# Kernel optimization log

Measured on AMD Instinct MI355X. Metric: run time of the kernel, lower is better.

Reference implementation:

```python
import jax, jax.numpy as jnp
import numpy as np

B, L, N, F, H, HOR = 32, 12, 1024, 2, 128, 12


def setup_inputs() -> dict:
    key = jax.random.key(0)
    ks = jax.random.split(key, 9)
    x = jax.random.normal(ks[0], (B, L, N, F), dtype=jnp.float32)
    # A_phys: sparse-ish binary physical adjacency, then normalize_adj: add self-loops, row-normalize
    A_phys = (jax.random.uniform(ks[1], (N, N)) < 0.05).astype(jnp.float32)
    A = A_phys + jnp.eye(N, dtype=jnp.float32)
    A = A / (A.sum(axis=1, keepdims=True) + 1e-6)
    # GraphGRUCell params (single layer): lin_x: F -> 3H, lin_h: H -> 3H
    sx = 1.0 / np.sqrt(F)
    sh = 1.0 / np.sqrt(H)
    W_x = jax.random.uniform(ks[2], (F, 3 * H), minval=-sx, maxval=sx)
    b_x = jax.random.uniform(ks[3], (3 * H,), minval=-sx, maxval=sx)
    W_h = jax.random.uniform(ks[4], (H, 3 * H), minval=-sh, maxval=sh)
    b_h = jax.random.uniform(ks[5], (3 * H,), minval=-sh, maxval=sh)
    # head: H -> horizon
    W_head = jax.random.uniform(ks[6], (H, HOR), minval=-sh, maxval=sh)
    b_head = jax.random.uniform(ks[7], (HOR,), minval=-sh, maxval=sh)
    return {"x": x, "A": A, "W_x": W_x, "b_x": b_x, "W_h": W_h, "b_h": b_h,
            "W_head": W_head, "b_head": b_head}


def reference(x, A, W_x, b_x, W_h, b_h, W_head, b_head):
    Bv, Lv, Nv, Fv = x.shape
    Hv = W_h.shape[0]

    def step(h, xt):
        # graph aggregation of hidden state: [N,N] x [B,N,H] -> [B,N,H]
        Ah = jnp.einsum('ij,bjh->bih', A, h)
        x_gates = xt @ W_x + b_x          # [B,N,3H]
        h_gates = Ah @ W_h + b_h          # [B,N,3H]
        z_x, r_x, n_x = jnp.split(x_gates, 3, axis=-1)
        z_h, r_h, n_h = jnp.split(h_gates, 3, axis=-1)
        z = jax.nn.sigmoid(z_x + z_h)
        r = jax.nn.sigmoid(r_x + r_h)
        n = jnp.tanh(n_x + r * n_h)
        h_new = (1.0 - z) * n + z * h
        return h_new, None

    h0 = jnp.zeros((Bv, Nv, Hv), dtype=x.dtype)
    xs = jnp.moveaxis(x, 1, 0)  # [L,B,N,F]
    h, _ = jax.lax.scan(step, h0, xs)
    y = (h @ W_head + b_head).transpose(0, 2, 1)  # [B, horizon, N]
    return y
```

## Files before the change

### kernel.cpp

```cpp
#include <hip/hip_runtime.h>
#include <hip/hip_bf16.h>

#define BB 32
#define LL 12
#define NN 1024
#define HH 128
#define HORN 12
#define G3 384

typedef unsigned short u16;
typedef unsigned int u32;
typedef unsigned long long u64;
typedef __attribute__((ext_vector_type(8))) short short8;
typedef __attribute__((ext_vector_type(4))) float f32x4;

__device__ __forceinline__ u16 to_bf16(float f) {
    return __builtin_bit_cast(u16, __float2bfloat16(f));
}
__device__ __forceinline__ float bf_to_f(u32 bits) {
    return __builtin_bit_cast(float, bits << 16);
}
__device__ __forceinline__ void gl16(const u16* g, char* l) {
    __builtin_amdgcn_global_load_lds((const __attribute__((address_space(1))) u32*)g,
                                     (__attribute__((address_space(3))) u32*)l, 16, 0, 0);
}

__global__ void prep_abf(const float* __restrict__ A, u16* __restrict__ Abf) {
    int t = blockIdx.x * blockDim.x + threadIdx.x;
    float4 v = ((const float4*)A)[t];
    ushort4 o;
    o.x = to_bf16(v.x); o.y = to_bf16(v.y); o.z = to_bf16(v.z); o.w = to_bf16(v.w);
    ((ushort4*)Abf)[t] = o;
}

__global__ void prep_whT(const float* __restrict__ W_h, u16* __restrict__ whT) {
    int t = blockIdx.x * blockDim.x + threadIdx.x;
    if (t >= HH * G3) return;
    int c = t / HH, k = t % HH;
    whT[c * HH + k] = to_bf16(W_h[k * G3 + c]);
}

template <bool FIRST, bool LAST>
__global__ __launch_bounds__(256, 3) void gru_step(
    const u16* __restrict__ Abf, const u16* __restrict__ hT_old,
    u16* __restrict__ hT_new, const u16* __restrict__ whT,
    const float* __restrict__ x, const float* __restrict__ W_x,
    const float* __restrict__ b_x, const float* __restrict__ b_h,
    const float* __restrict__ W_head, const float* __restrict__ b_head,
    float* __restrict__ out, int t) {
    __shared__ __align__(16) char smem[49152];

    int bid = blockIdx.x;
    int swz = (bid & 7) * 64 + (bid >> 3);
    int b = swz >> 4;
    int i0 = (swz & 15) * 64;
    int tid = threadIdx.x;
    int w = tid >> 6, lane = tid & 63;
    int lcol = lane & 15, kgrp = lane >> 4;
    int wm = w >> 1, wn = w & 1;
    u32 swzl = (u32)((lcol & 7) << 4);
    u32 a_b = (u32)((wm * 32 + lcol) * 128);
    u32 b_b = (u32)(8192 + (wn * 64 + lcol) * 128);

    f32x4 acc[2][4];
#pragma unroll
    for (int m = 0; m < 2; ++m)
#pragma unroll
        for (int n = 0; n < 4; ++n) acc[m][n] = (f32x4){0.f, 0.f, 0.f, 0.f};
    u64 hreg[2][4] = {{0, 0, 0, 0}, {0, 0, 0, 0}};

    if (!FIRST) {
        int lr3 = lane >> 3, lc8 = lane & 7;
        const u16* ag[2]; u32 al[2];
        const u16* bg[4]; u32 bl[4];
#pragma unroll
        for (int q = 0; q < 2; ++q) {
            int r = w * 16 + q * 8 + lr3;
            ag[q] = Abf + (size_t)(i0 + r) * 1024 + (lc8 ^ (r & 7)) * 8;
            al[q] = (u32)(w * 2048 + q * 1024);
        }
#pragma unroll
        for (int q = 0; q < 4; ++q) {
            int r = w * 32 + q * 8 + lr3;
            bg[q] = hT_old + (size_t)b * 131072 + (size_t)r * 1024 + (lc8 ^ (r & 7)) * 8;
            bl[q] = (u32)(8192 + w * 4096 + q * 1024);
        }

#pragma unroll
        for (int q = 0; q < 2; ++q) gl16(ag[q], smem + al[q]);
#pragma unroll
        for (int q = 0; q < 4; ++q) gl16(bg[q], smem + bl[q]);
#pragma unroll
        for (int q = 0; q < 2; ++q) gl16(ag[q] + 64, smem + 24576 + al[q]);
#pragma unroll
        for (int q = 0; q < 4; ++q) gl16(bg[q] + 64, smem + 24576 + bl[q]);

        int cstar = i0 >> 6;
        for (int c = 0; c < 16; ++c) {
            u32 sb = (u32)((c & 1) * 24576);
            if (c < 15) asm volatile("s_waitcnt vmcnt(6)" ::: "memory");
            else        asm volatile("s_waitcnt vmcnt(0)" ::: "memory");
            __builtin_amdgcn_s_barrier();
            __builtin_amdgcn_sched_barrier(0);

            if (c == cstar) {
#pragma unroll
                for (int sub = 0; sub < 2; ++sub) {
                    int hh = w * 32 + sub * 16 + lcol;
                    u32 rb = sb + 8192u + (u32)(hh * 128);
                    u32 sw = (u32)((hh & 7) << 4);
#pragma unroll
                    for (int rt = 0; rt < 4; ++rt)
                        hreg[sub][rt] = *(const u64*)(smem + rb + (((u32)(rt * 32 + kgrp * 8)) ^ sw));
                }
                asm volatile("s_waitcnt lgkmcnt(0)" ::: "memory");
                __builtin_amdgcn_sched_barrier(0);
            }

            __builtin_amdgcn_s_setprio(1);
#pragma unroll
            for (int ks = 0; ks < 2; ++ks) {
                u32 kb = ((u32)(ks * 64 + kgrp * 16)) ^ swzl;
                short8 a0 = *(const short8*)(smem + sb + a_b + kb);
                short8 a1 = *(const short8*)(smem + sb + a_b + 2048 + kb);
                short8 b0 = *(const short8*)(smem + sb + b_b + kb);
                short8 b1 = *(const short8*)(smem + sb + b_b + 2048 + kb);
                short8 b2 = *(const short8*)(smem + sb + b_b + 4096 + kb);
                short8 b3 = *(const short8*)(smem + sb + b_b + 6144 + kb);
                acc[0][0] = __builtin_amdgcn_mfma_f32_16x16x32_bf16(a0, b0, acc[0][0], 0, 0, 0);
                acc[0][1] = __builtin_amdgcn_mfma_f32_16x16x32_bf16(a0, b1, acc[0][1], 0, 0, 0);
                acc[0][2] = __builtin_amdgcn_mfma_f32_16x16x32_bf16(a0, b2, acc[0][2], 0, 0, 0);
                acc[0][3] = __builtin_amdgcn_mfma_f32_16x16x32_bf16(a0, b3, acc[0][3], 0, 0, 0);
                acc[1][0] = __builtin_amdgcn_mfma_f32_16x16x32_bf16(a1, b0, acc[1][0], 0, 0, 0);
                acc[1][1] = __builtin_amdgcn_mfma_f32_16x16x32_bf16(a1, b1, acc[1][1], 0, 0, 0);
                acc[1][2] = __builtin_amdgcn_mfma_f32_16x16x32_bf16(a1, b2, acc[1][2], 0, 0, 0);
                acc[1][3] = __builtin_amdgcn_mfma_f32_16x16x32_bf16(a1, b3, acc[1][3], 0, 0, 0);
            }
            __builtin_amdgcn_s_setprio(0);
            asm volatile("" ::: "memory");
            __builtin_amdgcn_s_barrier();
            if (c < 14) {
                int o = (c + 2) * 64;
#pragma unroll
                for (int q = 0; q < 2; ++q) gl16(ag[q] + o, smem + sb + al[q]);
#pragma unroll
                for (int q = 0; q < 4; ++q) gl16(bg[q] + o, smem + sb + bl[q]);
            }
        }
        asm volatile("" ::: "memory");
        __builtin_amdgcn_s_barrier();
    }

#pragma unroll
    for (int m = 0; m < 2; ++m)
#pragma unroll
        for (int n = 0; n < 4; ++n)
#pragma unroll
            for (int ri = 0; ri < 4; ++ri) {
                int row = wm * 32 + m * 16 + kgrp * 4 + ri;
                int col = wn * 64 + n * 16 + lcol;
                *(u16*)(smem + row * 256 + (((u32)(2 * col)) ^ ((u32)(row & 7) << 4))) =
                    to_bf16(acc[m][n][ri]);
            }
    __syncthreads();

#pragma unroll
    for (int sub = 0; sub < 2; ++sub) {
        int hh = w * 32 + sub * 16 + lcol;
        short8 bw[3][4];
#pragma unroll
        for (int g = 0; g < 3; ++g)
#pragma unroll
            for (int ks = 0; ks < 4; ++ks)
                bw[g][ks] = *(const short8*)(whT + (size_t)(g * 128 + hh) * 128 + ks * 32 + kgrp * 8);

        f32x4 acc2[4][3];
#pragma unroll
        for (int rt = 0; rt < 4; ++rt)
#pragma unroll
            for (int g = 0; g < 3; ++g) acc2[rt][g] = (f32x4){0.f, 0.f, 0.f, 0.f};

        __builtin_amdgcn_s_setprio(1);
#pragma unroll
        for (int rt = 0; rt < 4; ++rt) {
            u32 ab2 = (u32)((rt * 16 + lcol) * 256);
#pragma unroll
            for (int ks = 0; ks < 4; ++ks) {
                short8 a2 = *(const short8*)(smem + ab2 + (((u32)(ks * 64 + kgrp * 16)) ^ swzl));
                acc2[rt][0] = __builtin_amdgcn_mfma_f32_16x16x32_bf16(a2, bw[0][ks], acc2[rt][0], 0, 0, 0);
                acc2[rt][1] = __builtin_amdgcn_mfma_f32_16x16x32_bf16(a2, bw[1][ks], acc2[rt][1], 0, 0, 0);
                acc2[rt][2] = __builtin_amdgcn_mfma_f32_16x16x32_bf16(a2, bw[2][ks], acc2[rt][2], 0, 0, 0);
            }
        }
        __builtin_amdgcn_s_setprio(0);

        float bxz = b_x[hh], bxr = b_x[128 + hh], bxn = b_x[256 + hh];
        float bhz = b_h[hh], bhr = b_h[128 + hh], bhn = b_h[256 + hh];
        float wx0z = W_x[hh], wx0r = W_x[128 + hh], wx0n = W_x[256 + hh];
        float wx1z = W_x[G3 + hh], wx1r = W_x[G3 + 128 + hh], wx1n = W_x[G3 + 256 + hh];
#pragma unroll
        for (int rt = 0; rt < 4; ++rt) {
            u64 h4 = hreg[sub][rt];
#pragma unroll
            for (int ri = 0; ri < 4; ++ri) {
                int rl = rt * 16 + kgrp * 4 + ri;
                int i = i0 + rl;
                const float* xp = x + ((size_t)(b * LL + t) * NN + i) * 2;
                float x0 = xp[0], x1 = xp[1];
                float zin = acc2[rt][0][ri] + bhz + fmaf(x0, wx0z, fmaf(x1, wx1z, bxz));
                float rin = acc2[rt][1][ri] + bhr + fmaf(x0, wx0r, fmaf(x1, wx1r, bxr));
                float z = 1.f / (1.f + __expf(-zin));
                float rg = 1.f / (1.f + __expf(-rin));
                float nin = fmaf(rg, acc2[rt][2][ri] + bhn, fmaf(x0, wx0n, fmaf(x1, wx1n, bxn)));
                nin = fmaxf(nin, -40.f);
                float e = __expf(-2.f * nin);
                float n = (1.f - e) / (1.f + e);
                float hold = bf_to_f((u32)((h4 >> (16 * ri)) & 0xffffu));
                float hv = fmaf(z, hold - n, n);
                *(u16*)(smem + 16384 + hh * 128 + (((u32)(2 * rl)) ^ ((u32)(hh & 7) << 4))) = to_bf16(hv);
            }
        }
    }
    __syncthreads();

    if (!LAST) {
#pragma unroll
        for (int c2 = 0; c2 < 4; ++c2) {
            int o = c2 * 4096 + tid * 16;
            int nr = o >> 7, cb = o & 127;
            uint4 v = *(const uint4*)(smem + 16384 + nr * 128 + (((u32)cb) ^ ((u32)(nr & 7) << 4)));
            *(uint4*)((char*)(hT_new + (size_t)b * 131072 + (size_t)nr * 1024 + i0) + cb) = v;
        }
    } else {
        float* wl = (float*)(smem + 32768);
        float* blh = (float*)(smem + 38912);
        for (int ix = tid; ix < HH * HORN; ix += 256) wl[ix] = W_head[ix];
        if (tid < HORN) blh[tid] = b_head[tid];
        __syncthreads();
        int il = tid & 63, hg = tid >> 6;
        float a0 = blh[hg], a1 = blh[hg + 4], a2 = blh[hg + 8];
        for (int hh = 0; hh < 128; ++hh) {
            float hv = bf_to_f((u32)*(const u16*)(smem + 16384 + hh * 128 + (((u32)(2 * il)) ^ ((u32)(hh & 7) << 4))));
            a0 = fmaf(hv, wl[hh * HORN + hg], a0);
            a1 = fmaf(hv, wl[hh * HORN + hg + 4], a1);
            a2 = fmaf(hv, wl[hh * HORN + hg + 8], a2);
        }
        out[(size_t)(b * HORN + hg) * NN + i0 + il] = a0;
        out[(size_t)(b * HORN + hg + 4) * NN + i0 + il] = a1;
        out[(size_t)(b * HORN + hg + 8) * NN + i0 + il] = a2;
    }
}

extern "C" void kernel_launch(void* const* d_in, const int* in_sizes, int n_in,
                              void* d_out, int out_size, void* d_ws, size_t ws_size,
                              hipStream_t stream) {
    const float* x = (const float*)d_in[0];
    const float* A = (const float*)d_in[1];
    const float* W_x = (const float*)d_in[2];
    const float* b_x = (const float*)d_in[3];
    const float* W_h = (const float*)d_in[4];
    const float* b_h = (const float*)d_in[5];
    const float* W_head = (const float*)d_in[6];
    const float* b_head = (const float*)d_in[7];
    float* out = (float*)d_out;
    char* ws = (char*)d_ws;

    u16* hT0 = (u16*)(ws + 0);
    u16* hT1 = (u16*)(ws + 8388608);
    u16* Abf = (u16*)(ws + 16777216);
    u16* whT = (u16*)(ws + 18874368);

    prep_abf<<<1024, 256, 0, stream>>>(A, Abf);
    prep_whT<<<(HH * G3 + 255) / 256, 256, 0, stream>>>(W_h, whT);

    gru_step<true, false><<<512, 256, 0, stream>>>(Abf, hT1, hT0, whT, x, W_x, b_x, b_h,
                                                   W_head, b_head, out, 0);
    u16* hTo = hT0; u16* hTn = hT1;
    for (int t = 1; t < LL - 1; ++t) {
        gru_step<false, false><<<512, 256, 0, stream>>>(Abf, hTo, hTn, whT, x, W_x, b_x, b_h,
                                                        W_head, b_head, out, t);
        u16* tmp = hTo; hTo = hTn; hTn = tmp;
    }
    gru_step<false, true><<<512, 256, 0, stream>>>(Abf, hTo, hTn, whT, x, W_x, b_x, b_h,
                                                   W_head, b_head, out, LL - 1);
}
```

Baseline: 307.3 us.

## Double the row tile per block to 128 nodes, halving grid size

Each block now covers 128 node rows instead of 64 for one batch element. The per-block A-times-h GEMM becomes 128x128 with a 4x4 MFMA fragment per wave, which halves re-reading of each h_old slice across blocks and doubles MFMA work per LDS load. Shared memory grows to 64KB, launch bounds drop to one block per SM, and the grid shrinks from 512 to 256 blocks. The gate epilogue and head are split into two halves to match. The risk is that 256 blocks may underfill the GPU's compute units and that the lower occupancy may hide latency less well.

```diff
diff --git a/kernel.cpp b/kernel.cpp
--- a/kernel.cpp
+++ b/kernel.cpp
@@ -41,64 +41,56 @@
 }
 
 template <bool FIRST, bool LAST>
-__global__ __launch_bounds__(256, 3) void gru_step(
+__global__ __launch_bounds__(256, 1) void gru_step(
     const u16* __restrict__ Abf, const u16* __restrict__ hT_old,
     u16* __restrict__ hT_new, const u16* __restrict__ whT,
     const float* __restrict__ x, const float* __restrict__ W_x,
     const float* __restrict__ b_x, const float* __restrict__ b_h,
     const float* __restrict__ W_head, const float* __restrict__ b_head,
     float* __restrict__ out, int t) {
-    __shared__ __align__(16) char smem[49152];
+    __shared__ __align__(16) char smem[65536];
 
     int bid = blockIdx.x;
-    int swz = (bid & 7) * 64 + (bid >> 3);
-    int b = swz >> 4;
-    int i0 = (swz & 15) * 64;
+    int swz = (bid & 7) * 32 + (bid >> 3);
+    int b = swz >> 3;
+    int i0 = (swz & 7) * 128;
     int tid = threadIdx.x;
     int w = tid >> 6, lane = tid & 63;
     int lcol = lane & 15, kgrp = lane >> 4;
     int wm = w >> 1, wn = w & 1;
     u32 swzl = (u32)((lcol & 7) << 4);
-    u32 a_b = (u32)((wm * 32 + lcol) * 128);
-    u32 b_b = (u32)(8192 + (wn * 64 + lcol) * 128);
-
-    f32x4 acc[2][4];
-#pragma unroll
-    for (int m = 0; m < 2; ++m)
+    u32 a_b = (u32)((wm * 64 + lcol) * 128);
+    u32 b_b = (u32)(16384 + (wn * 64 + lcol) * 128);
+
+    f32x4 acc[4][4];
+#pragma unroll
+    for (int m = 0; m < 4; ++m)
 #pragma unroll
         for (int n = 0; n < 4; ++n) acc[m][n] = (f32x4){0.f, 0.f, 0.f, 0.f};
-    u64 hreg[2][4] = {{0, 0, 0, 0}, {0, 0, 0, 0}};
+    u64 hreg[2][2][4] = {};
 
     if (!FIRST) {
         int lr3 = lane >> 3, lc8 = lane & 7;
-        const u16* ag[2]; u32 al[2];
+        const u16* ag[4]; u32 al[4];
         const u16* bg[4]; u32 bl[4];
-#pragma unroll
-        for (int q = 0; q < 2; ++q) {
-            int r = w * 16 + q * 8 + lr3;
-            ag[q] = Abf + (size_t)(i0 + r) * 1024 + (lc8 ^ (r & 7)) * 8;
-            al[q] = (u32)(w * 2048 + q * 1024);
-        }
 #pragma unroll
         for (int q = 0; q < 4; ++q) {
             int r = w * 32 + q * 8 + lr3;
+            ag[q] = Abf + (size_t)(i0 + r) * 1024 + (lc8 ^ (r & 7)) * 8;
+            al[q] = (u32)(w * 4096 + q * 1024);
             bg[q] = hT_old + (size_t)b * 131072 + (size_t)r * 1024 + (lc8 ^ (r & 7)) * 8;
-            bl[q] = (u32)(8192 + w * 4096 + q * 1024);
-        }
-
-#pragma unroll
-        for (int q = 0; q < 2; ++q) gl16(ag[q], smem + al[q]);
-#pragma unroll
-        for (int q = 0; q < 4; ++q) gl16(bg[q], smem + bl[q]);
-#pragma unroll
-        for (int q = 0; q < 2; ++q) gl16(ag[q] + 64, smem + 24576 + al[q]);
-#pragma unroll
-        for (int q = 0; q < 4; ++q) gl16(bg[q] + 64, smem + 24576 + bl[q]);
+            bl[q] = (u32)(16384 + w * 4096 + q * 1024);
+        }
+
+#pragma unroll
+        for (int q = 0; q < 4; ++q) { gl16(ag[q], smem + al[q]); gl16(bg[q], smem + bl[q]); }
+#pragma unroll
+        for (int q = 0; q < 4; ++q) { gl16(ag[q] + 64, smem + 32768 + al[q]); gl16(bg[q] + 64, smem + 32768 + bl[q]); }
 
         int cstar = i0 >> 6;
         for (int c = 0; c < 16; ++c) {
-            u32 sb = (u32)((c & 1) * 24576);
-            if (c < 15) asm volatile("s_waitcnt vmcnt(6)" ::: "memory");
+            u32 sb = (u32)((c & 1) * 32768);
+            if (c < 15) asm volatile("s_waitcnt vmcnt(8)" ::: "memory");
             else        asm volatile("s_waitcnt vmcnt(0)" ::: "memory");
             __builtin_amdgcn_s_barrier();
             __builtin_amdgcn_sched_barrier(0);
@@ -107,34 +99,45 @@
 #pragma unroll
                 for (int sub = 0; sub < 2; ++sub) {
                     int hh = w * 32 + sub * 16 + lcol;
-                    u32 rb = sb + 8192u + (u32)(hh * 128);
+                    u32 rb = sb + 16384u + (u32)(hh * 128);
                     u32 sw = (u32)((hh & 7) << 4);
 #pragma unroll
                     for (int rt = 0; rt < 4; ++rt)
-                        hreg[sub][rt] = *(const u64*)(smem + rb + (((u32)(rt * 32 + kgrp * 8)) ^ sw));
+                        hreg[0][sub][rt] = *(const u64*)(smem + rb + (((u32)(rt * 32 + kgrp * 8)) ^ sw));
                 }
                 asm volatile("s_waitcnt lgkmcnt(0)" ::: "memory");
                 __builtin_amdgcn_sched_barrier(0);
             }
+            if (c == cstar + 1) {
+#pragma unroll
+                for (int sub = 0; sub < 2; ++sub) {
+                    int hh = w * 32 + sub * 16 + lcol;
+                    u32 rb = sb + 16384u + (u32)(hh * 128);
+                    u32 sw = (u32)((hh & 7) << 4);
+#pragma unroll
+                    for (int rt = 0; rt < 4; ++rt)
+                        hreg[1][sub][rt] = *(const u64*)(smem + rb + (((u32)(rt * 32 + kgrp * 8)) ^ sw));
+                }
+                asm volatile("s_waitcnt lgkmcnt(0)" ::: "memory");
+                __builtin_amdgcn_sched_barrier(0);
+            }
 
             __builtin_amdgcn_s_setprio(1);
 #pragma unroll
             for (int ks = 0; ks < 2; ++ks) {
                 u32 kb = ((u32)(ks * 64 + kgrp * 16)) ^ swzl;
-                short8 a0 = *(const short8*)(smem + sb + a_b + kb);
-                short8 a1 = *(const short8*)(smem + sb + a_b + 2048 + kb);
-                short8 b0 = *(const short8*)(smem + sb + b_b + kb);
-                short8 b1 = *(const short8*)(smem + sb + b_b + 2048 + kb);
-                short8 b2 = *(const short8*)(smem + sb + b_b + 4096 + kb);
-                short8 b3 = *(const short8*)(smem + sb + b_b + 6144 + kb);
-                acc[0][0] = __builtin_amdgcn_mfma_f32_16x16x32_bf16(a0, b0, acc[0][0], 0, 0, 0);
-                acc[0][1] = __builtin_amdgcn_mfma_f32_16x16x32_bf16(a0, b1, acc[0][1], 0, 0, 0);
-                acc[0][2] = __builtin_amdgcn_mfma_f32_16x16x32_bf16(a0, b2, acc[0][2], 0, 0, 0);
-                acc[0][3] = __builtin_amdgcn_mfma_f32_16x16x32_bf16(a0, b3, acc[0][3], 0, 0, 0);
-                acc[1][0] = __builtin_amdgcn_mfma_f32_16x16x32_bf16(a1, b0, acc[1][0], 0, 0, 0);
-                acc[1][1] = __builtin_amdgcn_mfma_f32_16x16x32_bf16(a1, b1, acc[1][1], 0, 0, 0);
-                acc[1][2] = __builtin_amdgcn_mfma_f32_16x16x32_bf16(a1, b2, acc[1][2], 0, 0, 0);
-                acc[1][3] = __builtin_amdgcn_mfma_f32_16x16x32_bf16(a1, b3, acc[1][3], 0, 0, 0);
+                short8 af[4], bf[4];
+#pragma unroll
+                for (int m = 0; m < 4; ++m)
+                    af[m] = *(const short8*)(smem + sb + a_b + (u32)(m * 2048) + kb);
+#pragma unroll
+                for (int n = 0; n < 4; ++n)
+                    bf[n] = *(const short8*)(smem + sb + b_b + (u32)(n * 2048) + kb);
+#pragma unroll
+                for (int m = 0; m < 4; ++m)
+#pragma unroll
+                    for (int n = 0; n < 4; ++n)
+                        acc[m][n] = __builtin_amdgcn_mfma_f32_16x16x32_bf16(af[m], bf[n], acc[m][n], 0, 0, 0);
             }
             __builtin_amdgcn_s_setprio(0);
             asm volatile("" ::: "memory");
@@ -142,9 +145,7 @@
             if (c < 14) {
                 int o = (c + 2) * 64;
 #pragma unroll
-                for (int q = 0; q < 2; ++q) gl16(ag[q] + o, smem + sb + al[q]);
-#pragma unroll
-                for (int q = 0; q < 4; ++q) gl16(bg[q] + o, smem + sb + bl[q]);
+                for (int q = 0; q < 4; ++q) { gl16(ag[q] + o, smem + sb + al[q]); gl16(bg[q] + o, smem + sb + bl[q]); }
             }
         }
         asm volatile("" ::: "memory");
@@ -152,12 +153,12 @@
     }
 
 #pragma unroll
-    for (int m = 0; m < 2; ++m)
+    for (int m = 0; m < 4; ++m)
 #pragma unroll
         for (int n = 0; n < 4; ++n)
 #pragma unroll
             for (int ri = 0; ri < 4; ++ri) {
-                int row = wm * 32 + m * 16 + kgrp * 4 + ri;
+                int row = wm * 64 + m * 16 + kgrp * 4 + ri;
                 int col = wn * 64 + n * 16 + lcol;
                 *(u16*)(smem + row * 256 + (((u32)(2 * col)) ^ ((u32)(row & 7) << 4))) =
                     to_bf16(acc[m][n][ri]);
@@ -173,51 +174,55 @@
 #pragma unroll
             for (int ks = 0; ks < 4; ++ks)
                 bw[g][ks] = *(const short8*)(whT + (size_t)(g * 128 + hh) * 128 + ks * 32 + kgrp * 8);
-
-        f32x4 acc2[4][3];
-#pragma unroll
-        for (int rt = 0; rt < 4; ++rt)
-#pragma unroll
-            for (int g = 0; g < 3; ++g) acc2[rt][g] = (f32x4){0.f, 0.f, 0.f, 0.f};
-
-        __builtin_amdgcn_s_setprio(1);
-#pragma unroll
-        for (int rt = 0; rt < 4; ++rt) {
-            u32 ab2 = (u32)((rt * 16 + lcol) * 256);
-#pragma unroll
-            for (int ks = 0; ks < 4; ++ks) {
-                short8 a2 = *(const short8*)(smem + ab2 + (((u32)(ks * 64 + kgrp * 16)) ^ swzl));
-                acc2[rt][0] = __builtin_amdgcn_mfma_f32_16x16x32_bf16(a2, bw[0][ks], acc2[rt][0], 0, 0, 0);
-                acc2[rt][1] = __builtin_amdgcn_mfma_f32_16x16x32_bf16(a2, bw[1][ks], acc2[rt][1], 0, 0, 0);
-                acc2[rt][2] = __builtin_amdgcn_mfma_f32_16x16x32_bf16(a2, bw[2][ks], acc2[rt][2], 0, 0, 0);
-            }
-        }
-        __builtin_amdgcn_s_setprio(0);
 
         float bxz = b_x[hh], bxr = b_x[128 + hh], bxn = b_x[256 + hh];
         float bhz = b_h[hh], bhr = b_h[128 + hh], bhn = b_h[256 + hh];
         float wx0z = W_x[hh], wx0r = W_x[128 + hh], wx0n = W_x[256 + hh];
         float wx1z = W_x[G3 + hh], wx1r = W_x[G3 + 128 + hh], wx1n = W_x[G3 + 256 + hh];
-#pragma unroll
-        for (int rt = 0; rt < 4; ++rt) {
-            u64 h4 = hreg[sub][rt];
-#pragma unroll
-            for (int ri = 0; ri < 4; ++ri) {
-                int rl = rt * 16 + kgrp * 4 + ri;
-                int i = i0 + rl;
-                const float* xp = x + ((size_t)(b * LL + t) * NN + i) * 2;
-                float x0 = xp[0], x1 = xp[1];
-                float zin = acc2[rt][0][ri] + bhz + fmaf(x0, wx0z, fmaf(x1, wx1z, bxz));
-                float rin = acc2[rt][1][ri] + bhr + fmaf(x0, wx0r, fmaf(x1, wx1r, bxr));
-                float z = 1.f / (1.f + __expf(-zin));
-                float rg = 1.f / (1.f + __expf(-rin));
-                float nin = fmaf(rg, acc2[rt][2][ri] + bhn, fmaf(x0, wx0n, fmaf(x1, wx1n, bxn)));
-                nin = fmaxf(nin, -40.f);
-                float e = __expf(-2.f * nin);
-                float n = (1.f - e) / (1.f + e);
-                float hold = bf_to_f((u32)((h4 >> (16 * ri)) & 0xffffu));
-                float hv = fmaf(z, hold - n, n);
-                *(u16*)(smem + 16384 + hh * 128 + (((u32)(2 * rl)) ^ ((u32)(hh & 7) << 4))) = to_bf16(hv);
+
+#pragma unroll
+        for (int half = 0; half < 2; ++half) {
+            f32x4 acc2[4][3];
+#pragma unroll
+            for (int rt = 0; rt < 4; ++rt)
+#pragma unroll
+                for (int g = 0; g < 3; ++g) acc2[rt][g] = (f32x4){0.f, 0.f, 0.f, 0.f};
+
+            __builtin_amdgcn_s_setprio(1);
+#pragma unroll
+            for (int rt = 0; rt < 4; ++rt) {
+                u32 ab2 = (u32)((half * 64 + rt * 16 + lcol) * 256);
+#pragma unroll
+                for (int ks = 0; ks < 4; ++ks) {
+                    short8 a2 = *(const short8*)(smem + ab2 + (((u32)(ks * 64 + kgrp * 16)) ^ swzl));
+                    acc2[rt][0] = __builtin_amdgcn_mfma_f32_16x16x32_bf16(a2, bw[0][ks], acc2[rt][0], 0, 0, 0);
+                    acc2[rt][1] = __builtin_amdgcn_mfma_f32_16x16x32_bf16(a2, bw[1][ks], acc2[rt][1], 0, 0, 0);
+                    acc2[rt][2] = __builtin_amdgcn_mfma_f32_16x16x32_bf16(a2, bw[2][ks], acc2[rt][2], 0, 0, 0);
+                }
+            }
+            __builtin_amdgcn_s_setprio(0);
+
+#pragma unroll
+            for (int rt = 0; rt < 4; ++rt) {
+                u64 h4 = hreg[half][sub][rt];
+#pragma unroll
+                for (int ri = 0; ri < 4; ++ri) {
+                    int rl = half * 64 + rt * 16 + kgrp * 4 + ri;
+                    int i = i0 + rl;
+                    const float* xp = x + ((size_t)(b * LL + t) * NN + i) * 2;
+                    float x0 = xp[0], x1 = xp[1];
+                    float zin = acc2[rt][0][ri] + bhz + fmaf(x0, wx0z, fmaf(x1, wx1z, bxz));
+                    float rin = acc2[rt][1][ri] + bhr + fmaf(x0, wx0r, fmaf(x1, wx1r, bxr));
+                    float z = 1.f / (1.f + __expf(-zin));
+                    float rg = 1.f / (1.f + __expf(-rin));
+                    float nin = fmaf(rg, acc2[rt][2][ri] + bhn, fmaf(x0, wx0n, fmaf(x1, wx1n, bxn)));
+                    nin = fmaxf(nin, -40.f);
+                    float e = __expf(-2.f * nin);
+                    float n = (1.f - e) / (1.f + e);
+                    float hold = bf_to_f((u32)((h4 >> (16 * ri)) & 0xffffu));
+                    float hv = fmaf(z, hold - n, n);
+                    *(u16*)(smem + 32768 + hh * 256 + (((u32)(2 * rl)) ^ ((u32)(hh & 7) << 4))) = to_bf16(hv);
+                }
             }
         }
     }
@@ -225,29 +230,30 @@
 
     if (!LAST) {
 #pragma unroll
-        for (int c2 = 0; c2 < 4; ++c2) {
+        for (int c2 = 0; c2 < 8; ++c2) {
             int o = c2 * 4096 + tid * 16;
-            int nr = o >> 7, cb = o & 127;
-            uint4 v = *(const uint4*)(smem + 16384 + nr * 128 + (((u32)cb) ^ ((u32)(nr & 7) << 4)));
+            int nr = o >> 8, cb = o & 255;
+            uint4 v = *(const uint4*)(smem + 32768 + nr * 256 + (((u32)cb) ^ ((u32)(nr & 7) << 4)));
             *(uint4*)((char*)(hT_new + (size_t)b * 131072 + (size_t)nr * 1024 + i0) + cb) = v;
         }
     } else {
-        float* wl = (float*)(smem + 32768);
-        float* blh = (float*)(smem + 38912);
+        float* wl = (float*)smem;
+        float* blh = (float*)(smem + 6144);
         for (int ix = tid; ix < HH * HORN; ix += 256) wl[ix] = W_head[ix];
         if (tid < HORN) blh[tid] = b_head[tid];
         __syncthreads();
-        int il = tid & 63, hg = tid >> 6;
-        float a0 = blh[hg], a1 = blh[hg + 4], a2 = blh[hg + 8];
+        int il = tid & 127, grp = tid >> 7;
+        float a[6];
+#pragma unroll
+        for (int j = 0; j < 6; ++j) a[j] = blh[grp * 6 + j];
         for (int hh = 0; hh < 128; ++hh) {
-            float hv = bf_to_f((u32)*(const u16*)(smem + 16384 + hh * 128 + (((u32)(2 * il)) ^ ((u32)(hh & 7) << 4))));
-            a0 = fmaf(hv, wl[hh * HORN + hg], a0);
-            a1 = fmaf(hv, wl[hh * HORN + hg + 4], a1);
-            a2 = fmaf(hv, wl[hh * HORN + hg + 8], a2);
-        }
-        out[(size_t)(b * HORN + hg) * NN + i0 + il] = a0;
-        out[(size_t)(b * HORN + hg + 4) * NN + i0 + il] = a1;
-        out[(size_t)(b * HORN + hg + 8) * NN + i0 + il] = a2;
+            float hv = bf_to_f((u32)*(const u16*)(smem + 32768 + hh * 256 + (((u32)(2 * il)) ^ ((u32)(hh & 7) << 4))));
+#pragma unroll
+            for (int j = 0; j < 6; ++j) a[j] = fmaf(hv, wl[hh * HORN + grp * 6 + j], a[j]);
+        }
+#pragma unroll
+        for (int j = 0; j < 6; ++j)
+            out[(size_t)(b * HORN + grp * 6 + j) * NN + i0 + il] = a[j];
     }
 }
 
@@ -273,14 +279,14 @@
     prep_abf<<<1024, 256, 0, stream>>>(A, Abf);
     prep_whT<<<(HH * G3 + 255) / 256, 256, 0, stream>>>(W_h, whT);
 
-    gru_step<true, false><<<512, 256, 0, stream>>>(Abf, hT1, hT0, whT, x, W_x, b_x, b_h,
+    gru_step<true, false><<<256, 256, 0, stream>>>(Abf, hT1, hT0, whT, x, W_x, b_x, b_h,
                                                    W_head, b_head, out, 0);
     u16* hTo = hT0; u16* hTn = hT1;
     for (int t = 1; t < LL - 1; ++t) {
-        gru_step<false, false><<<512, 256, 0, stream>>>(Abf, hTo, hTn, whT, x, W_x, b_x, b_h,
+        gru_step<false, false><<<256, 256, 0, stream>>>(Abf, hTo, hTn, whT, x, W_x, b_x, b_h,
                                                         W_head, b_head, out, t);
         u16* tmp = hTo; hTo = hTn; hTn = tmp;
     }
-    gru_step<false, true><<<512, 256, 0, stream>>>(Abf, hTo, hTn, whT, x, W_x, b_x, b_h,
+    gru_step<false, true><<<256, 256, 0, stream>>>(Abf, hTo, hTn, whT, x, W_x, b_x, b_h,
                                                    W_head, b_head, out, LL - 1);
 }
```

Result: slower. 352.1 us (+14.6%).
